# Kernel optimization log

Measured on AMD Instinct MI355X. Metric: run time of the kernel, lower is better.

Reference implementation:

```python
import jax, jax.numpy as jnp
import numpy as np

S, N, K, B = 4, 16384, 128, 131072  # num_sim, nodes, k_dim, num pairs


def setup_inputs() -> dict:
    key = jax.random.key(0)
    ks = jax.random.split(key, 16)
    sc = 0.05
    return {
        "X": jax.random.normal(ks[0], (S, N, K), jnp.float32),
        "Y": jax.random.normal(ks[1], (S, N, K), jnp.float32),
        "x_att": jax.random.normal(ks[2], (S,), jnp.float32),
        "y_att": jax.random.normal(ks[3], (S,), jnp.float32),
        "W_cX1": jax.random.normal(ks[4], (S * K, 1), jnp.float32) * sc,
        "b_cX1": jnp.zeros((1,), jnp.float32),
        "W_cX2": jax.random.normal(ks[5], (1, K), jnp.float32) * sc,
        "b_cX2": jnp.zeros((K,), jnp.float32),
        "W_cY1": jax.random.normal(ks[6], (S * K, 1), jnp.float32) * sc,
        "b_cY1": jnp.zeros((1,), jnp.float32),
        "W_cY2": jax.random.normal(ks[7], (1, K), jnp.float32) * sc,
        "b_cY2": jnp.zeros((K,), jnp.float32),
        "W0": jax.random.normal(ks[8], (2 * K, K), jnp.float32) * sc,
        "b0": jnp.zeros((K,), jnp.float32),
        "W1": jax.random.normal(ks[9], (K, K // 2), jnp.float32) * sc,
        "b1": jnp.zeros((K // 2,), jnp.float32),
        "W2": jax.random.normal(ks[10], (K // 2, 1), jnp.float32) * sc,
        "b2": jnp.zeros((1,), jnp.float32),
        "idx0": jax.random.randint(ks[11], (B,), 0, N, jnp.int32),
        "idx1": jax.random.randint(ks[12], (B,), 0, N, jnp.int32),
    }


def _embed(Z, idx, att_vec, Wc1, bc1, Wc2, bc2):
    """0.5 * (sim_5 + sim_8) embedding for one side. Z: [S,N,K], idx: [B]."""
    lrelu = jax.nn.leaky_relu  # negative_slope=0.01, matches torch default
    Zs = jnp.transpose(Z[:, idx, :], (1, 0, 2))            # [B, S, K]
    Zsum = Zs.sum(axis=1)                                   # [B, K]
    # sim_5: concat views -> scalar -> K attention, softmax over K
    Zcat = Zs.reshape(Zs.shape[0], -1)                      # [B, S*K]
    att = jax.nn.softmax(lrelu(Zcat @ Wc1 + bc1) @ Wc2 + bc2, axis=-1)
    e5 = Zsum * att                                         # [B, K]
    # sim_8: softmax-weighted sum over views
    e8 = jnp.einsum('bsk,s->bk', Zs, jax.nn.softmax(att_vec))
    return 0.5 * (e5 + e8)


def reference(X, Y, x_att, y_att,
              W_cX1, b_cX1, W_cX2, b_cX2,
              W_cY1, b_cY1, W_cY2, b_cY2,
              W0, b0, W1, b1, W2, b2,
              idx0, idx1):
    lrelu = jax.nn.leaky_relu
    X_embed = _embed(X, idx0, x_att, W_cX1, b_cX1, W_cX2, b_cX2)  # [B, K]
    Y_embed = _embed(Y, idx1, y_att, W_cY1, b_cY1, W_cY2, b_cY2)  # [B, K]
    # get_pred, score_type='cat': decoder0 -> decoder1 -> decoder2 -> sigmoid
    feat = jnp.concatenate([X_embed, Y_embed], axis=1)             # [B, 2K]
    o = lrelu(feat @ W0 + b0)                                      # [B, K]
    o = lrelu(o @ W1 + b1)                                         # [B, K/2]
    pred = (o @ W2 + b2).ravel()                                   # [B]
    return jax.nn.sigmoid(pred)
```

## Files before the change

### kernel.cpp

```cpp
#include <hip/hip_runtime.h>
#include <hip/hip_bf16.h>

#define S_   4
#define N_   16384
#define K_   128
#define CONV_BLOCKS 160

typedef __attribute__((ext_vector_type(8))) short short8v;
typedef __attribute__((ext_vector_type(4))) float f32x4;

__device__ __forceinline__ float lrelu(float x) { return x > 0.f ? x : 0.01f * x; }

__device__ __forceinline__ unsigned short f2bf(float f) {
    union { float f; unsigned u; } v; v.f = f;
    unsigned r = v.u + 0x7fff + ((v.u >> 16) & 1);
    return (unsigned short)(r >> 16);
}

__global__ __launch_bounds__(256)
void embed_convert(const float* __restrict__ X, const float* __restrict__ Y,
                   const float* __restrict__ x_att, const float* __restrict__ y_att,
                   const float* __restrict__ WcX1, const float* __restrict__ bcX1,
                   const float* __restrict__ WcX2, const float* __restrict__ bcX2,
                   const float* __restrict__ WcY1, const float* __restrict__ bcY1,
                   const float* __restrict__ WcY2, const float* __restrict__ bcY2,
                   const float* __restrict__ W0, const float* __restrict__ W1,
                   unsigned short* __restrict__ W0T, unsigned short* __restrict__ W1T,
                   unsigned short* __restrict__ Xemb, unsigned short* __restrict__ Yemb)
{
    if (blockIdx.x < CONV_BLOCKS) {
        int t = blockIdx.x * 256 + threadIdx.x;
        if (t < 128 * 256) {
            int n = t >> 8, k = t & 255;
            W0T[t] = f2bf(W0[k * 128 + n]);
        }
        t -= 128 * 256;
        if (t >= 0 && t < 64 * 128) {
            int n = t >> 7, k = t & 127;
            W1T[t] = f2bf(W1[k * 64 + n]);
        }
        return;
    }

    const int node = (blockIdx.x - CONV_BLOCKS) * 4 + (threadIdx.x >> 6);
    if (node >= N_) return;
    const int lane = threadIdx.x & 63;
    const int half = lane >> 5;
    const int sl   = lane & 31;
    const int k0   = sl * 4;

    const float* Z    = half ? Y    : X;
    const float* Wc1  = half ? WcY1 : WcX1;
    const float* Wc2  = half ? WcY2 : WcX2;
    const float* bc2h = half ? bcY2 : bcX2;
    const float  bc1v = half ? bcY1[0] : bcX1[0];
    const float* attv = half ? y_att : x_att;
    unsigned short* dst = half ? Yemb : Xemb;

    float a0 = attv[0], a1 = attv[1], a2 = attv[2], a3 = attv[3];
    float am = fmaxf(fmaxf(a0, a1), fmaxf(a2, a3));
    float sw0 = __expf(a0 - am), sw1 = __expf(a1 - am),
          sw2 = __expf(a2 - am), sw3 = __expf(a3 - am);
    float swinv = 1.f / (sw0 + sw1 + sw2 + sw3);
    sw0 *= swinv; sw1 *= swinv; sw2 *= swinv; sw3 *= swinv;

    float4 z0 = *(const float4*)(Z + ((size_t)0 * N_ + node) * K_ + k0);
    float4 z1 = *(const float4*)(Z + ((size_t)1 * N_ + node) * K_ + k0);
    float4 z2 = *(const float4*)(Z + ((size_t)2 * N_ + node) * K_ + k0);
    float4 z3 = *(const float4*)(Z + ((size_t)3 * N_ + node) * K_ + k0);
    float4 w0 = *(const float4*)(Wc1 + 0 * K_ + k0);
    float4 w1 = *(const float4*)(Wc1 + 1 * K_ + k0);
    float4 w2 = *(const float4*)(Wc1 + 2 * K_ + k0);
    float4 w3 = *(const float4*)(Wc1 + 3 * K_ + k0);
    float4 c2 = *(const float4*)(Wc2 + k0);
    float4 cb = *(const float4*)(bc2h + k0);

    float4 zs;
    zs.x = z0.x + z1.x + z2.x + z3.x;
    zs.y = z0.y + z1.y + z2.y + z3.y;
    zs.z = z0.z + z1.z + z2.z + z3.z;
    zs.w = z0.w + z1.w + z2.w + z3.w;

    float dp = z0.x*w0.x + z0.y*w0.y + z0.z*w0.z + z0.w*w0.w
             + z1.x*w1.x + z1.y*w1.y + z1.z*w1.z + z1.w*w1.w
             + z2.x*w2.x + z2.y*w2.y + z2.z*w2.z + z2.w*w2.w
             + z3.x*w3.x + z3.y*w3.y + z3.z*w3.z + z3.w*w3.w;
#pragma unroll
    for (int off = 16; off >= 1; off >>= 1) dp += __shfl_xor(dp, off, 64);

    float a = lrelu(dp + bc1v);

    float l0 = fmaf(a, c2.x, cb.x), l1 = fmaf(a, c2.y, cb.y);
    float l2 = fmaf(a, c2.z, cb.z), l3 = fmaf(a, c2.w, cb.w);
    float m = fmaxf(fmaxf(l0, l1), fmaxf(l2, l3));
#pragma unroll
    for (int off = 16; off >= 1; off >>= 1) m = fmaxf(m, __shfl_xor(m, off, 64));
    float e0 = __expf(l0 - m), e1 = __expf(l1 - m),
          e2 = __expf(l2 - m), e3 = __expf(l3 - m);
    float s = e0 + e1 + e2 + e3;
#pragma unroll
    for (int off = 16; off >= 1; off >>= 1) s += __shfl_xor(s, off, 64);
    float inv = 1.f / s;

    float o0v = 0.5f * (zs.x * (e0 * inv) + (sw0*z0.x + sw1*z1.x + sw2*z2.x + sw3*z3.x));
    float o1v = 0.5f * (zs.y * (e1 * inv) + (sw0*z0.y + sw1*z1.y + sw2*z2.y + sw3*z3.y));
    float o2v = 0.5f * (zs.z * (e2 * inv) + (sw0*z0.z + sw1*z1.z + sw2*z2.z + sw3*z3.z));
    float o3v = 0.5f * (zs.w * (e3 * inv) + (sw0*z0.w + sw1*z1.w + sw2*z2.w + sw3*z3.w));

    ushort4 p;
    p.x = f2bf(o0v); p.y = f2bf(o1v); p.z = f2bf(o2v); p.w = f2bf(o3v);
    *(ushort4*)(dst + (size_t)node * K_ + k0) = p;
}

__global__ __launch_bounds__(256, 4)
void decoder_kernel(const unsigned short* __restrict__ Xemb,
                    const unsigned short* __restrict__ Yemb,
                    const unsigned short* __restrict__ W0T,
                    const unsigned short* __restrict__ W1T,
                    const float* __restrict__ b0, const float* __restrict__ b1,
                    const float* __restrict__ W2, const float* __restrict__ b2,
                    const int* __restrict__ idx0, const int* __restrict__ idx1,
                    float* __restrict__ out, int Btot)
{
    __shared__ unsigned short o0[128 * 136];

    const int wave = threadIdx.x >> 6;
    const int lane = threadIdx.x & 63;
    const int lx   = lane & 15;
    const int lk   = lane >> 4;
    const int rowBase = blockIdx.x * 128 + wave * 32;

    int r0 = rowBase + lx;       if (r0 >= Btot) r0 = Btot - 1;
    int r1 = rowBase + 16 + lx;  if (r1 >= Btot) r1 = Btot - 1;
    const unsigned short* xb0 = Xemb + (size_t)idx0[r0] * K_ + lk * 8;
    const unsigned short* xb1 = Xemb + (size_t)idx0[r1] * K_ + lk * 8;
    const unsigned short* yb0 = Yemb + (size_t)idx1[r0] * K_ + lk * 8;
    const unsigned short* yb1 = Yemb + (size_t)idx1[r1] * K_ + lk * 8;

    float b0v[8], b1v[4], w2v[4];
#pragma unroll
    for (int n = 0; n < 8; ++n) b0v[n] = b0[n * 16 + lx];
#pragma unroll
    for (int n = 0; n < 4; ++n) { b1v[n] = b1[n * 16 + lx]; w2v[n] = W2[n * 16 + lx]; }
    const float b2v = b2[0];

    short8v A0[8], A1[8];
#pragma unroll
    for (int kk = 0; kk < 4; ++kk) {
        A0[kk]     = *(const short8v*)(xb0 + kk * 32);
        A1[kk]     = *(const short8v*)(xb1 + kk * 32);
        A0[kk + 4] = *(const short8v*)(yb0 + kk * 32);
        A1[kk + 4] = *(const short8v*)(yb1 + kk * 32);
    }

    f32x4 acc[2][8];
#pragma unroll
    for (int m = 0; m < 2; ++m)
#pragma unroll
        for (int n = 0; n < 8; ++n) acc[m][n] = (f32x4)0.f;

#pragma unroll
    for (int kk = 0; kk < 8; ++kk) {
        const int koff = kk * 32 + lk * 8;
        short8v Bv[8];
#pragma unroll
        for (int n = 0; n < 8; ++n)
            Bv[n] = *(const short8v*)(W0T + (size_t)(n * 16 + lx) * 256 + koff);
#pragma unroll
        for (int n = 0; n < 8; ++n) {
            acc[0][n] = __builtin_amdgcn_mfma_f32_16x16x32_bf16(A0[kk], Bv[n], acc[0][n], 0, 0, 0);
            acc[1][n] = __builtin_amdgcn_mfma_f32_16x16x32_bf16(A1[kk], Bv[n], acc[1][n], 0, 0, 0);
        }
    }

#pragma unroll
    for (int m = 0; m < 2; ++m)
#pragma unroll
        for (int n = 0; n < 8; ++n)
#pragma unroll
            for (int r = 0; r < 4; ++r) {
                float v = lrelu(acc[m][n][r] + b0v[n]);
                int row = wave * 32 + m * 16 + lk * 4 + r;
                o0[row * 136 + n * 16 + lx] = f2bf(v);
            }

    short8v La0[4], La1[4];
#pragma unroll
    for (int kk = 0; kk < 4; ++kk) {
        const int koff = kk * 32 + lk * 8;
        La0[kk] = *(const short8v*)(&o0[(wave * 32 + lx) * 136 + koff]);
        La1[kk] = *(const short8v*)(&o0[(wave * 32 + 16 + lx) * 136 + koff]);
    }

    f32x4 acc1[2][4];
#pragma unroll
    for (int m = 0; m < 2; ++m)
#pragma unroll
        for (int n = 0; n < 4; ++n) acc1[m][n] = (f32x4)0.f;

#pragma unroll
    for (int kk = 0; kk < 4; ++kk) {
        const int koff = kk * 32 + lk * 8;
        short8v Bv1[4];
#pragma unroll
        for (int n = 0; n < 4; ++n)
            Bv1[n] = *(const short8v*)(W1T + (size_t)(n * 16 + lx) * 128 + koff);
#pragma unroll
        for (int n = 0; n < 4; ++n) {
            acc1[0][n] = __builtin_amdgcn_mfma_f32_16x16x32_bf16(La0[kk], Bv1[n], acc1[0][n], 0, 0, 0);
            acc1[1][n] = __builtin_amdgcn_mfma_f32_16x16x32_bf16(La1[kk], Bv1[n], acc1[1][n], 0, 0, 0);
        }
    }

    {
        float t[2][4];
#pragma unroll
        for (int m = 0; m < 2; ++m)
#pragma unroll
            for (int r = 0; r < 4; ++r) t[m][r] = 0.f;
#pragma unroll
        for (int m = 0; m < 2; ++m)
#pragma unroll
            for (int n = 0; n < 4; ++n)
#pragma unroll
                for (int r = 0; r < 4; ++r) {
                    float v = lrelu(acc1[m][n][r] + b1v[n]);
                    t[m][r] = fmaf(v, w2v[n], t[m][r]);
                }
#pragma unroll
        for (int off = 8; off >= 1; off >>= 1)
#pragma unroll
            for (int m = 0; m < 2; ++m)
#pragma unroll
                for (int r = 0; r < 4; ++r)
                    t[m][r] += __shfl_xor(t[m][r], off, 64);
        if (lx == 0) {
#pragma unroll
            for (int m = 0; m < 2; ++m)
#pragma unroll
                for (int r = 0; r < 4; ++r) {
                    int row = rowBase + m * 16 + lk * 4 + r;
                    if (row < Btot)
                        out[row] = 1.f / (1.f + __expf(-(t[m][r] + b2v)));
                }
        }
    }
}

#define PPB  32
#define NT   256
#define FSTR 260
#define O0STR 132
#define O1STR 68

__device__ __forceinline__ void embed_side_f(
    const float* __restrict__ Z, int idx,
    const float* __restrict__ Wc1, float bc1v,
    const float* __restrict__ Wc2, const float* __restrict__ bc2,
    float sw0, float sw1, float sw2, float sw3,
    int lane, float* dst)
{
    const int k0 = 2 * lane;
    const float* base = Z + (size_t)idx * K_ + k0;
    float2 z0 = *(const float2*)(base + (size_t)0 * N_ * K_);
    float2 z1 = *(const float2*)(base + (size_t)1 * N_ * K_);
    float2 z2 = *(const float2*)(base + (size_t)2 * N_ * K_);
    float2 z3 = *(const float2*)(base + (size_t)3 * N_ * K_);
    float zs0 = z0.x + z1.x + z2.x + z3.x;
    float zs1 = z0.y + z1.y + z2.y + z3.y;
    float2 w0 = *(const float2*)(Wc1 + 0 * K_ + k0);
    float2 w1 = *(const float2*)(Wc1 + 1 * K_ + k0);
    float2 w2 = *(const float2*)(Wc1 + 2 * K_ + k0);
    float2 w3 = *(const float2*)(Wc1 + 3 * K_ + k0);
    float dp = z0.x*w0.x + z0.y*w0.y + z1.x*w1.x + z1.y*w1.y
             + z2.x*w2.x + z2.y*w2.y + z3.x*w3.x + z3.y*w3.y;
#pragma unroll
    for (int off = 32; off >= 1; off >>= 1) dp += __shfl_xor(dp, off, 64);
    float a = lrelu(dp + bc1v);
    float2 c2 = *(const float2*)(Wc2 + k0);
    float2 cb = *(const float2*)(bc2 + k0);
    float l0 = fmaf(a, c2.x, cb.x), l1 = fmaf(a, c2.y, cb.y);
    float m = fmaxf(l0, l1);
#pragma unroll
    for (int off = 32; off >= 1; off >>= 1) m = fmaxf(m, __shfl_xor(m, off, 64));
    float e0 = __expf(l0 - m), e1 = __expf(l1 - m);
    float s = e0 + e1;
#pragma unroll
    for (int off = 32; off >= 1; off >>= 1) s += __shfl_xor(s, off, 64);
    float inv = 1.f / s;
    float e8a = sw0*z0.x + sw1*z1.x + sw2*z2.x + sw3*z3.x;
    float e8b = sw0*z0.y + sw1*z1.y + sw2*z2.y + sw3*z3.y;
    *(float2*)(dst + k0) = make_float2(0.5f*(zs0*(e0*inv)+e8a), 0.5f*(zs1*(e1*inv)+e8b));
}

__global__ __launch_bounds__(NT)
void mf_fused(const float* __restrict__ X, const float* __restrict__ Y,
              const float* __restrict__ x_att, const float* __restrict__ y_att,
              const float* __restrict__ WcX1, const float* __restrict__ bcX1,
              const float* __restrict__ WcX2, const float* __restrict__ bcX2,
              const float* __restrict__ WcY1, const float* __restrict__ bcY1,
              const float* __restrict__ WcY2, const float* __restrict__ bcY2,
              const float* __restrict__ W0, const float* __restrict__ b0,
              const float* __restrict__ W1, const float* __restrict__ b1,
              const float* __restrict__ W2, const float* __restrict__ b2,
              const int* __restrict__ idx0, const int* __restrict__ idx1,
              float* __restrict__ out, int Btot)
{
    __shared__ float pool[PPB * FSTR];
    float* feat = pool;
    const int tid  = threadIdx.x;
    const int lane = tid & 63;
    const int wave = tid >> 6;
    float swx0, swx1, swx2, swx3, swy0, swy1, swy2, swy3;
    {
        float a0 = x_att[0], a1 = x_att[1], a2 = x_att[2], a3 = x_att[3];
        float m = fmaxf(fmaxf(a0, a1), fmaxf(a2, a3));
        float e0 = __expf(a0-m), e1 = __expf(a1-m), e2 = __expf(a2-m), e3 = __expf(a3-m);
        float inv = 1.f / (e0+e1+e2+e3);
        swx0=e0*inv; swx1=e1*inv; swx2=e2*inv; swx3=e3*inv;
        float b0v=y_att[0], b1v=y_att[1], b2v=y_att[2], b3v=y_att[3];
        float my = fmaxf(fmaxf(b0v,b1v), fmaxf(b2v,b3v));
        float f0=__expf(b0v-my), f1=__expf(b1v-my), f2=__expf(b2v-my), f3=__expf(b3v-my);
        float invy = 1.f/(f0+f1+f2+f3);
        swy0=f0*invy; swy1=f1*invy; swy2=f2*invy; swy3=f3*invy;
    }
    const float bcX1v = bcX1[0], bcY1v = bcY1[0];
    const long pair_base = (long)blockIdx.x * PPB;
    for (int pp = 0; pp < PPB/4; ++pp) {
        const int p_local = wave * (PPB/4) + pp;
        const long pair = pair_base + p_local;
        if (pair < Btot) {
            embed_side_f(X, idx0[pair], WcX1, bcX1v, WcX2, bcX2, swx0,swx1,swx2,swx3, lane, feat + p_local*FSTR);
            embed_side_f(Y, idx1[pair], WcY1, bcY1v, WcY2, bcY2, swy0,swy1,swy2,swy3, lane, feat + p_local*FSTR + K_);
        }
    }
    __syncthreads();
    const int jg = tid & 15, pg = tid >> 4;
    float acc[2][8];
#pragma unroll
    for (int p=0;p<2;++p)
#pragma unroll
        for (int j=0;j<8;++j) acc[p][j]=0.f;
    const float* frow0 = feat + (pg*2+0)*FSTR;
    const float* frow1 = feat + (pg*2+1)*FSTR;
    for (int i = 0; i < 2*K_; i += 4) {
        float fav[4], fbv[4];
        *(float4*)fav = *(const float4*)(frow0+i);
        *(float4*)fbv = *(const float4*)(frow1+i);
#pragma unroll
        for (int u=0;u<4;++u) {
            float wv[8];
            *(float4*)(wv)   = *(const float4*)(W0 + (i+u)*K_ + jg*8);
            *(float4*)(wv+4) = *(const float4*)(W0 + (i+u)*K_ + jg*8 + 4);
#pragma unroll
            for (int j=0;j<8;++j) {
                acc[0][j] = fmaf(fav[u], wv[j], acc[0][j]);
                acc[1][j] = fmaf(fbv[u], wv[j], acc[1][j]);
            }
        }
    }
    __syncthreads();
    float* o0 = pool;
    {
        float bv[8];
        *(float4*)bv     = *(const float4*)(b0 + jg*8);
        *(float4*)(bv+4) = *(const float4*)(b0 + jg*8 + 4);
#pragma unroll
        for (int p=0;p<2;++p) {
            float v[8];
#pragma unroll
            for (int j=0;j<8;++j) v[j] = lrelu(acc[p][j] + bv[j]);
            *(float4*)(o0 + (pg*2+p)*O0STR + jg*8)     = *(float4*)v;
            *(float4*)(o0 + (pg*2+p)*O0STR + jg*8 + 4) = *(float4*)(v+4);
        }
    }
    __syncthreads();
    float acc1[2][4];
#pragma unroll
    for (int p=0;p<2;++p)
#pragma unroll
        for (int j=0;j<4;++j) acc1[p][j]=0.f;
    const float* r0 = o0 + (pg*2+0)*O0STR;
    const float* r1 = o0 + (pg*2+1)*O0STR;
    for (int i = 0; i < K_; i += 4) {
        float fav[4], fbv[4];
        *(float4*)fav = *(const float4*)(r0+i);
        *(float4*)fbv = *(const float4*)(r1+i);
#pragma unroll
        for (int u=0;u<4;++u) {
            float wv[4];
            *(float4*)wv = *(const float4*)(W1 + (i+u)*(K_/2) + jg*4);
#pragma unroll
            for (int j=0;j<4;++j) {
                acc1[0][j] = fmaf(fav[u], wv[j], acc1[0][j]);
                acc1[1][j] = fmaf(fbv[u], wv[j], acc1[1][j]);
            }
        }
    }
    float* o1 = pool + PPB*O0STR;
    {
        float bv[4];
        *(float4*)bv = *(const float4*)(b1 + jg*4);
#pragma unroll
        for (int p=0;p<2;++p) {
            float v[4];
#pragma unroll
            for (int j=0;j<4;++j) v[j] = lrelu(acc1[p][j] + bv[j]);
            *(float4*)(o1 + (pg*2+p)*O1STR + jg*4) = *(float4*)v;
        }
    }
    __syncthreads();
    {
        const int p = tid >> 3, part = tid & 7;
        const float* r = o1 + p*O1STR + part*8;
        float rv[8], wv[8];
        *(float4*)rv     = *(const float4*)(r);
        *(float4*)(rv+4) = *(const float4*)(r+4);
        *(float4*)wv     = *(const float4*)(W2 + part*8);
        *(float4*)(wv+4) = *(const float4*)(W2 + part*8 + 4);
        float d = 0.f;
#pragma unroll
        for (int j=0;j<8;++j) d = fmaf(rv[j], wv[j], d);
        d += __shfl_xor(d, 1, 64);
        d += __shfl_xor(d, 2, 64);
        d += __shfl_xor(d, 4, 64);
        if (part == 0) {
            const long pair = pair_base + p;
            if (pair < Btot) out[pair] = 1.f / (1.f + __expf(-(d + b2[0])));
        }
    }
}

extern "C" void kernel_launch(void* const* d_in, const int* in_sizes, int n_in,
                              void* d_out, int out_size, void* d_ws, size_t ws_size,
                              hipStream_t stream) {
    const float* X    = (const float*)d_in[0];
    const float* Y    = (const float*)d_in[1];
    const float* xatt = (const float*)d_in[2];
    const float* yatt = (const float*)d_in[3];
    const float* WcX1 = (const float*)d_in[4];
    const float* bcX1 = (const float*)d_in[5];
    const float* WcX2 = (const float*)d_in[6];
    const float* bcX2 = (const float*)d_in[7];
    const float* WcY1 = (const float*)d_in[8];
    const float* bcY1 = (const float*)d_in[9];
    const float* WcY2 = (const float*)d_in[10];
    const float* bcY2 = (const float*)d_in[11];
    const float* W0   = (const float*)d_in[12];
    const float* b0   = (const float*)d_in[13];
    const float* W1   = (const float*)d_in[14];
    const float* b1   = (const float*)d_in[15];
    const float* W2   = (const float*)d_in[16];
    const float* b2   = (const float*)d_in[17];
    const int* idx0   = (const int*)d_in[18];
    const int* idx1   = (const int*)d_in[19];
    float* out        = (float*)d_out;

    const int Btot = in_sizes[18];
    const int dblocks = (Btot + 127) / 128;
    const size_t need = (9u << 20);

    if (ws_size >= need) {
        unsigned short* W0T  = (unsigned short*)d_ws;
        unsigned short* W1T  = (unsigned short*)((char*)d_ws + 65536);
        unsigned short* Xemb = (unsigned short*)((char*)d_ws + (1u << 20));
        unsigned short* Yemb = (unsigned short*)((char*)d_ws + (5u << 20));

        embed_convert<<<CONV_BLOCKS + N_ / 4, 256, 0, stream>>>(
            X, Y, xatt, yatt, WcX1, bcX1, WcX2, bcX2,
            WcY1, bcY1, WcY2, bcY2, W0, W1, W0T, W1T, Xemb, Yemb);
        decoder_kernel<<<dblocks, 256, 0, stream>>>(
            Xemb, Yemb, W0T, W1T, b0, b1, W2, b2, idx0, idx1, out, Btot);
    } else {
        mf_fused<<<(Btot + PPB - 1) / PPB, NT, 0, stream>>>(
            X, Y, xatt, yatt, WcX1, bcX1, WcX2, bcX2,
            WcY1, bcY1, WcY2, bcY2, W0, b0, W1, b1, W2, b2,
            idx0, idx1, out, Btot);
    }
}
```

Baseline: 180.5 us.

## Stage W0 in LDS by halves and fuse layer-1 MFMA per column chunk

The embed kernel now writes a padded (stride 272) bf16 image of W0 transposed. The decoder copies it into shared memory in two halves and reads W0 tiles from LDS, where before every wave read them straight from global memory. Layer 0 is computed one 16-column chunk at a time, and every two chunks the result goes to a small per-wave scratch buffer that feeds the layer-1 MFMAs. This removes the large 128x136 o0 buffer and many live accumulators, trading them for extra block syncs and cooperative LDS copies of about 35KB per half, with occupancy lowered to 3 blocks.

```diff
diff --git a/kernel.cpp b/kernel.cpp
--- a/kernel.cpp
+++ b/kernel.cpp
@@ -4,7 +4,12 @@
 #define S_   4
 #define N_   16384
 #define K_   128
-#define CONV_BLOCKS 160
+#define LDSTRIDE 272
+#define W0IMG_ELEMS (128 * LDSTRIDE)
+#define HALF_ELEMS  (64 * LDSTRIDE)
+#define SCR_STRIDE  40
+#define CONV_ELEMS  (W0IMG_ELEMS + 64 * 128)
+#define CONV_BLOCKS ((CONV_ELEMS + 255) / 256)
 
 typedef __attribute__((ext_vector_type(8))) short short8v;
 typedef __attribute__((ext_vector_type(4))) float f32x4;
@@ -25,16 +30,16 @@
                    const float* __restrict__ WcY1, const float* __restrict__ bcY1,
                    const float* __restrict__ WcY2, const float* __restrict__ bcY2,
                    const float* __restrict__ W0, const float* __restrict__ W1,
-                   unsigned short* __restrict__ W0T, unsigned short* __restrict__ W1T,
+                   unsigned short* __restrict__ W0img, unsigned short* __restrict__ W1T,
                    unsigned short* __restrict__ Xemb, unsigned short* __restrict__ Yemb)
 {
     if (blockIdx.x < CONV_BLOCKS) {
         int t = blockIdx.x * 256 + threadIdx.x;
-        if (t < 128 * 256) {
-            int n = t >> 8, k = t & 255;
-            W0T[t] = f2bf(W0[k * 128 + n]);
-        }
-        t -= 128 * 256;
+        if (t < W0IMG_ELEMS) {
+            int row = t / LDSTRIDE, col = t % LDSTRIDE;
+            W0img[t] = (col < 256) ? f2bf(W0[col * 128 + row]) : (unsigned short)0;
+        }
+        t -= W0IMG_ELEMS;
         if (t >= 0 && t < 64 * 128) {
             int n = t >> 7, k = t & 127;
             W1T[t] = f2bf(W1[k * 64 + n]);
@@ -112,23 +117,25 @@
     *(ushort4*)(dst + (size_t)node * K_ + k0) = p;
 }
 
-__global__ __launch_bounds__(256, 4)
+__global__ __launch_bounds__(256, 3)
 void decoder_kernel(const unsigned short* __restrict__ Xemb,
                     const unsigned short* __restrict__ Yemb,
-                    const unsigned short* __restrict__ W0T,
+                    const unsigned short* __restrict__ W0img,
                     const unsigned short* __restrict__ W1T,
                     const float* __restrict__ b0, const float* __restrict__ b1,
                     const float* __restrict__ W2, const float* __restrict__ b2,
                     const int* __restrict__ idx0, const int* __restrict__ idx1,
                     float* __restrict__ out, int Btot)
 {
-    __shared__ unsigned short o0[128 * 136];
+    __shared__ unsigned short Wlds[HALF_ELEMS];
+    __shared__ unsigned short scr[4][32 * SCR_STRIDE];
 
     const int wave = threadIdx.x >> 6;
     const int lane = threadIdx.x & 63;
     const int lx   = lane & 15;
     const int lk   = lane >> 4;
     const int rowBase = blockIdx.x * 128 + wave * 32;
+    unsigned short* myscr = scr[wave];
 
     int r0 = rowBase + lx;       if (r0 >= Btot) r0 = Btot - 1;
     int r1 = rowBase + 16 + lx;  if (r1 >= Btot) r1 = Btot - 1;
@@ -153,63 +160,60 @@
         A1[kk + 4] = *(const short8v*)(yb1 + kk * 32);
     }
 
-    f32x4 acc[2][8];
+    f32x4 acc1[2][4];
 #pragma unroll
     for (int m = 0; m < 2; ++m)
 #pragma unroll
-        for (int n = 0; n < 8; ++n) acc[m][n] = (f32x4)0.f;
-
-#pragma unroll
-    for (int kk = 0; kk < 8; ++kk) {
-        const int koff = kk * 32 + lk * 8;
-        short8v Bv[8];
-#pragma unroll
-        for (int n = 0; n < 8; ++n)
-            Bv[n] = *(const short8v*)(W0T + (size_t)(n * 16 + lx) * 256 + koff);
-#pragma unroll
-        for (int n = 0; n < 8; ++n) {
-            acc[0][n] = __builtin_amdgcn_mfma_f32_16x16x32_bf16(A0[kk], Bv[n], acc[0][n], 0, 0, 0);
-            acc[1][n] = __builtin_amdgcn_mfma_f32_16x16x32_bf16(A1[kk], Bv[n], acc[1][n], 0, 0, 0);
-        }
-    }
-
-#pragma unroll
-    for (int m = 0; m < 2; ++m)
-#pragma unroll
-        for (int n = 0; n < 8; ++n)
-#pragma unroll
-            for (int r = 0; r < 4; ++r) {
-                float v = lrelu(acc[m][n][r] + b0v[n]);
-                int row = wave * 32 + m * 16 + lk * 4 + r;
-                o0[row * 136 + n * 16 + lx] = f2bf(v);
+        for (int n = 0; n < 4; ++n) acc1[m][n] = (f32x4)0.f;
+
+#pragma unroll
+    for (int h = 0; h < 2; ++h) {
+        {
+            const unsigned short* src = W0img + h * HALF_ELEMS;
+#pragma unroll
+            for (int it = 0; it < 9; ++it) {
+                int e = it * 2048 + threadIdx.x * 8;
+                if (e < HALF_ELEMS)
+                    *(short8v*)&Wlds[e] = *(const short8v*)&src[e];
             }
-
-    short8v La0[4], La1[4];
-#pragma unroll
-    for (int kk = 0; kk < 4; ++kk) {
-        const int koff = kk * 32 + lk * 8;
-        La0[kk] = *(const short8v*)(&o0[(wave * 32 + lx) * 136 + koff]);
-        La1[kk] = *(const short8v*)(&o0[(wave * 32 + 16 + lx) * 136 + koff]);
-    }
-
-    f32x4 acc1[2][4];
-#pragma unroll
-    for (int m = 0; m < 2; ++m)
-#pragma unroll
-        for (int n = 0; n < 4; ++n) acc1[m][n] = (f32x4)0.f;
-
-#pragma unroll
-    for (int kk = 0; kk < 4; ++kk) {
-        const int koff = kk * 32 + lk * 8;
-        short8v Bv1[4];
-#pragma unroll
-        for (int n = 0; n < 4; ++n)
-            Bv1[n] = *(const short8v*)(W1T + (size_t)(n * 16 + lx) * 128 + koff);
-#pragma unroll
-        for (int n = 0; n < 4; ++n) {
-            acc1[0][n] = __builtin_amdgcn_mfma_f32_16x16x32_bf16(La0[kk], Bv1[n], acc1[0][n], 0, 0, 0);
-            acc1[1][n] = __builtin_amdgcn_mfma_f32_16x16x32_bf16(La1[kk], Bv1[n], acc1[1][n], 0, 0, 0);
-        }
+        }
+        __syncthreads();
+
+        for (int nl = 0; nl < 4; ++nl) {
+            const int n = h * 4 + nl;
+            const unsigned short* wb = Wlds + (nl * 16 + lx) * LDSTRIDE + lk * 8;
+
+            f32x4 accn[2];
+            accn[0] = (f32x4)0.f; accn[1] = (f32x4)0.f;
+#pragma unroll
+            for (int kk = 0; kk < 8; ++kk) {
+                short8v Bv = *(const short8v*)(wb + kk * 32);
+                accn[0] = __builtin_amdgcn_mfma_f32_16x16x32_bf16(A0[kk], Bv, accn[0], 0, 0, 0);
+                accn[1] = __builtin_amdgcn_mfma_f32_16x16x32_bf16(A1[kk], Bv, accn[1], 0, 0, 0);
+            }
+
+            const int ncol = (n & 1) * 16 + lx;
+#pragma unroll
+            for (int m = 0; m < 2; ++m)
+#pragma unroll
+                for (int r = 0; r < 4; ++r) {
+                    float v = lrelu(accn[m][r] + b0v[n]);
+                    myscr[(m * 16 + lk * 4 + r) * SCR_STRIDE + ncol] = f2bf(v);
+                }
+
+            if (n & 1) {
+                const int kk1 = n >> 1;
+                short8v La0 = *(const short8v*)&myscr[lx * SCR_STRIDE + lk * 8];
+                short8v La1 = *(const short8v*)&myscr[(16 + lx) * SCR_STRIDE + lk * 8];
+#pragma unroll
+                for (int n1 = 0; n1 < 4; ++n1) {
+                    short8v Bv1 = *(const short8v*)(W1T + (size_t)(n1 * 16 + lx) * 128 + kk1 * 32 + lk * 8);
+                    acc1[0][n1] = __builtin_amdgcn_mfma_f32_16x16x32_bf16(La0, Bv1, acc1[0][n1], 0, 0, 0);
+                    acc1[1][n1] = __builtin_amdgcn_mfma_f32_16x16x32_bf16(La1, Bv1, acc1[1][n1], 0, 0, 0);
+                }
+            }
+        }
+        __syncthreads();
     }
 
     {
@@ -461,16 +465,16 @@
     const size_t need = (9u << 20);
 
     if (ws_size >= need) {
-        unsigned short* W0T  = (unsigned short*)d_ws;
-        unsigned short* W1T  = (unsigned short*)((char*)d_ws + 65536);
-        unsigned short* Xemb = (unsigned short*)((char*)d_ws + (1u << 20));
-        unsigned short* Yemb = (unsigned short*)((char*)d_ws + (5u << 20));
+        unsigned short* W0img = (unsigned short*)d_ws;
+        unsigned short* W1T   = (unsigned short*)((char*)d_ws + 131072);
+        unsigned short* Xemb  = (unsigned short*)((char*)d_ws + (1u << 20));
+        unsigned short* Yemb  = (unsigned short*)((char*)d_ws + (5u << 20));
 
         embed_convert<<<CONV_BLOCKS + N_ / 4, 256, 0, stream>>>(
             X, Y, xatt, yatt, WcX1, bcX1, WcX2, bcX2,
-            WcY1, bcY1, WcY2, bcY2, W0, W1, W0T, W1T, Xemb, Yemb);
+            WcY1, bcY1, WcY2, bcY2, W0, W1, W0img, W1T, Xemb, Yemb);
         decoder_kernel<<<dblocks, 256, 0, stream>>>(
-            Xemb, Yemb, W0T, W1T, b0, b1, W2, b2, idx0, idx1, out, Btot);
+            Xemb, Yemb, W0img, W1T, b0, b1, W2, b2, idx0, idx1, out, Btot);
     } else {
         mf_fused<<<(Btot + PPB - 1) / PPB, NT, 0, stream>>>(
             X, Y, xatt, yatt, WcX1, bcX1, WcX2, bcX2,
```

Result: faster. 159.4 us (-11.7%).
